# Performance work log

Hardware: AMD Instinct MI355X
Metric: run time of the kernel (lower is better)

The kernel has to match this reference:

```python
import jax, jax.numpy as jnp
import numpy as np

NUM_CLASSES = 80
PRE_NMS_K = 400    # pre_nms_points / max_output_size_per_class
MAX_BOXES = 200    # max_total_size
NMS_THRESH = 0.6
SCORE_THRESH = 0.0  # iou_thresh in YoloLayer, used as score threshold/mask
SCALE_XY = (1.2, 1.1, 1.05)  # levels 3,4,5
STRIDES = (8.0, 16.0, 32.0)  # 2**level


def setup_inputs() -> dict:
    key = jax.random.key(0)
    k3, k4, k5 = jax.random.split(key, 3)
    B, C5 = 8, 3 * (NUM_CLASSES + 5)
    p3 = jax.random.normal(k3, (B, 64, 64, C5), dtype=jnp.float32)
    p4 = jax.random.normal(k4, (B, 32, 32, C5), dtype=jnp.float32)
    p5 = jax.random.normal(k5, (B, 16, 16, C5), dtype=jnp.float32)
    a3 = jnp.array([[12., 16.], [19., 36.], [40., 28.]], jnp.float32)
    a4 = jnp.array([[36., 75.], [76., 55.], [72., 146.]], jnp.float32)
    a5 = jnp.array([[142., 110.], [192., 243.], [459., 401.]], jnp.float32)
    return {"p3": p3, "p4": p4, "p5": p5, "a3": a3, "a4": a4, "a5": a5}


def _decode_level(p, anchors, stride, scale_xy):
    # p: [B,H,W,A*(C+5)] raw head output; 'original' box decode (sigmoid xy, exp wh)
    B, H, W, _ = p.shape
    A = anchors.shape[0]
    d = p.reshape(B, H, W, A, NUM_CLASSES + 5)
    txy, twh, tobj, tcls = d[..., :2], d[..., 2:4], d[..., 4:5], d[..., 5:]
    gx, gy = jnp.meshgrid(jnp.arange(W, dtype=p.dtype), jnp.arange(H, dtype=p.dtype))
    grid = jnp.stack([gx, gy], -1)[None, :, :, None, :]          # [1,H,W,1,2] (x,y)
    sxy = jnp.asarray(scale_xy, p.dtype)
    xy = (jax.nn.sigmoid(txy) * sxy - 0.5 * (sxy - 1.0) + grid) / jnp.array([W, H], p.dtype)
    wh = jnp.exp(twh) * anchors[None, None, None] / jnp.array([W * stride, H * stride], p.dtype)
    x1y1 = xy - 0.5 * wh
    x2y2 = xy + 0.5 * wh
    boxes = jnp.stack([x1y1[..., 1], x1y1[..., 0], x2y2[..., 1], x2y2[..., 0]], -1)  # yxyx
    obj = jax.nn.sigmoid(tobj)
    cls = jax.nn.sigmoid(tcls) * obj
    N = H * W * A
    return boxes.reshape(B, N, 4), cls.reshape(B, N, NUM_CLASSES), obj.reshape(B, N)


def _pairwise_iou(b):
    # b: [K,4] yxyx in [0,1]
    area = (b[:, 2] - b[:, 0]) * (b[:, 3] - b[:, 1])
    tl = jnp.maximum(b[:, None, :2], b[None, :, :2])
    br = jnp.minimum(b[:, None, 2:], b[None, :, 2:])
    wh = jnp.maximum(br - tl, 0.0)
    inter = wh[..., 0] * wh[..., 1]
    union = area[:, None] + area[None, :] - inter
    return inter / jnp.maximum(union, 1e-9)


def _greedy_nms_scores(boxes, scores):
    # boxes/scores already sorted by score descending; returns scores with suppressed -> 0
    K = scores.shape[0]
    overlap = _pairwise_iou(boxes) > NMS_THRESH
    idx = jnp.arange(K)

    def body(i, keep):
        sup = overlap[i] & (idx > i) & keep[i]
        return keep & ~sup

    keep = jax.lax.fori_loop(0, K, body, jnp.ones((K,), bool))
    return jnp.where(keep & (scores > SCORE_THRESH), scores, 0.0)


def _detections_per_image(boxes, cls_scores):
    # boxes [N,4], cls_scores [N,C] -> combined per-class NMS, top MAX_BOXES overall
    boxes = jnp.clip(boxes, 0.0, 1.0)  # combined NMS clips boxes by default

    def per_class(scores_c):
        vals, idx = jax.lax.top_k(scores_c, PRE_NMS_K)
        b = boxes[idx]
        return _greedy_nms_scores(b, vals), b

    kept_scores, kept_boxes = jax.vmap(per_class)(cls_scores.T)  # [C,K], [C,K,4]
    flat_s = kept_scores.reshape(-1)
    flat_b = kept_boxes.reshape(-1, 4)
    cls_ids = jnp.repeat(jnp.arange(NUM_CLASSES), PRE_NMS_K)
    top_s, top_i = jax.lax.top_k(flat_s, MAX_BOXES)
    top_b = flat_b[top_i]
    top_c = cls_ids[top_i].astype(jnp.float32)
    valid = top_s > 0.0
    top_b = jnp.where(valid[:, None], top_b, 0.0)
    top_c = jnp.where(valid, top_c, 0.0)
    num = jnp.sum(valid.astype(jnp.int32))
    return top_b, top_s, top_c, num


def _forward(p3, p4, p5, a3, a4, a5):
    boxes, cls_scores, obj_scores = [], [], []
    for (p, a), stride, sxy in zip(((p3, a3), (p4, a4), (p5, a5)), STRIDES, SCALE_XY):
        b, c, o = _decode_level(p, a, stride, sxy)
        boxes.append(b); cls_scores.append(c); obj_scores.append(o)
    boxes = jnp.concatenate(boxes, 1)            # [B,N,4]
    cls_scores = jnp.concatenate(cls_scores, 1)  # [B,N,C]
    obj_scores = jnp.concatenate(obj_scores, 1)  # [B,N]
    obj_mask = (obj_scores > SCORE_THRESH).astype(boxes.dtype)
    cls_mask = (cls_scores > SCORE_THRESH).astype(boxes.dtype)
    cls_scores = cls_scores * obj_mask[..., None] * cls_mask
    return jax.vmap(_detections_per_image)(boxes, cls_scores)


def reference(p3, p4, p5, a3, a4, a5):
    bbox, confidence, classes, num_detections = _forward(p3, p4, p5, a3, a4, a5)
    return bbox, confidence, classes, num_detections
```

## Files before the change

### kernel.cpp

```cpp
#include <hip/hip_runtime.h>
#include <math.h>

#define NCLS 80
#define PRE_K 400
#define MAX_BOXES 200
#define KEEP_CAP 200
#define N_TOT 16128
#define M_FIN (NCLS * KEEP_CAP)
#define NMS_T 0.6f
#define NTHR 1024
#define NWAVE (NTHR / 64)
#define FTHR 512
#define CAP 512

typedef unsigned long long u64;
typedef unsigned int u32;
typedef unsigned short u16;

__device__ __forceinline__ float sigf(float x) { return 1.0f / (1.0f + expf(-x)); }

__device__ __forceinline__ float score_f32(int idx, int b, int c,
    const float* __restrict__ p3, const float* __restrict__ p4, const float* __restrict__ p5)
{
    const float* base; int W, n;
    if (idx < 12288)      { base = p3; W = 64; n = idx; }
    else if (idx < 15360) { base = p4; W = 32; n = idx - 12288; }
    else                  { base = p5; W = 16; n = idx - 15360; }
    int a = n % 3, hw = n / 3, w = hw % W, h = hw / W;
    const float* rec = base + (((b * W + h) * W + w) * 255 + a * 85);
    return sigf(rec[5 + c]) * sigf(rec[4]);
}

__device__ __forceinline__ void hist_agg(u32* hist, u32 d, bool valid, int lane)
{
    u64 act = __ballot(valid);
    while (act) {
        int ldr = __ffsll((unsigned long long)act) - 1;
        u32 dl = __shfl(d, ldr, 64);
        u64 m = __ballot(valid && d == dl);
        if (lane == ldr) atomicAdd(&hist[dl], (u32)__popcll(m));
        act &= ~m;
    }
}

__device__ __forceinline__ void digit_select(const u32* hist, int need,
                                             u32* sh_dg, u32* sh_S1, u32* sh_T, int tid)
{
    if (tid < 64) {
        const int lane = tid;
        u32 h0 = hist[4 * lane + 0], h1 = hist[4 * lane + 1];
        u32 h2 = hist[4 * lane + 2], h3 = hist[4 * lane + 3];
        u32 loc = h0 + h1 + h2 + h3;
        u32 s = loc;
#pragma unroll
        for (int off = 1; off < 64; off <<= 1) {
            u32 t = __shfl_down(s, off, 64);
            if (lane + off < 64) s += t;
        }
        u32 after = s - loc;
        u32 S3 = h3 + after, S2 = h2 + S3, S1v = h1 + S2, S0 = h0 + S1v;
        u32 Sarr[5] = { S0, S1v, S2, S3, after };
#pragma unroll
        for (int k = 0; k < 4; ++k) {
            if ((int)Sarr[k] >= need && need > (int)Sarr[k + 1]) {
                *sh_dg = (u32)(4 * lane + k);
                *sh_S1 = Sarr[k + 1];
                *sh_T  = Sarr[k] - Sarr[k + 1];
            }
        }
    }
    __syncthreads();
}

__device__ __forceinline__ void sort512(u64* cand, int tid)
{
    u64 v = cand[tid];
#pragma unroll
    for (int k2 = 2; k2 <= 64; k2 <<= 1) {
#pragma unroll
        for (int j = k2 >> 1; j > 0; j >>= 1) {
            u64 p = __shfl_xor(v, j, 64);
            bool takeMax = ((tid & k2) == 0) ^ ((tid & j) != 0);
            v = takeMax ? (v >= p ? v : p) : (v <= p ? v : p);
        }
    }
    for (int k2 = 128; k2 <= CAP; k2 <<= 1) {
        for (int j = k2 >> 1; j >= 64; j >>= 1) {
            __syncthreads();
            cand[tid] = v;
            __syncthreads();
            u64 p = cand[tid ^ j];
            bool takeMax = ((tid & k2) == 0) ^ ((tid & j) != 0);
            v = takeMax ? (v >= p ? v : p) : (v <= p ? v : p);
        }
#pragma unroll
        for (int j = 32; j > 0; j >>= 1) {
            u64 p = __shfl_xor(v, j, 64);
            bool takeMax = ((tid & k2) == 0) ^ ((tid & j) != 0);
            v = takeMax ? (v >= p ? v : p) : (v <= p ? v : p);
        }
    }
    __syncthreads();
    cand[tid] = v;
    __syncthreads();
}

__device__ __forceinline__ void sort512_wide(u64* cand, int tid)
{
    u64 v = 0ull;
    if (tid < 512) {
        v = cand[tid];
#pragma unroll
        for (int k2 = 2; k2 <= 64; k2 <<= 1) {
#pragma unroll
            for (int j = k2 >> 1; j > 0; j >>= 1) {
                u64 p = __shfl_xor(v, j, 64);
                bool takeMax = ((tid & k2) == 0) ^ ((tid & j) != 0);
                v = takeMax ? (v >= p ? v : p) : (v <= p ? v : p);
            }
        }
    }
    for (int k2 = 128; k2 <= CAP; k2 <<= 1) {
        for (int j = k2 >> 1; j >= 64; j >>= 1) {
            __syncthreads();
            if (tid < 512) cand[tid] = v;
            __syncthreads();
            if (tid < 512) {
                u64 p = cand[tid ^ j];
                bool takeMax = ((tid & k2) == 0) ^ ((tid & j) != 0);
                v = takeMax ? (v >= p ? v : p) : (v <= p ? v : p);
            }
        }
        if (tid < 512) {
#pragma unroll
            for (int j = 32; j > 0; j >>= 1) {
                u64 p = __shfl_xor(v, j, 64);
                bool takeMax = ((tid & k2) == 0) ^ ((tid & j) != 0);
                v = takeMax ? (v >= p ? v : p) : (v <= p ? v : p);
            }
        }
    }
    __syncthreads();
    if (tid < 512) cand[tid] = v;
    __syncthreads();
}

__global__ __launch_bounds__(256) void decode_kernel(
    const float* __restrict__ p3, const float* __restrict__ p4, const float* __restrict__ p5,
    const float* __restrict__ a3, const float* __restrict__ a4, const float* __restrict__ a5,
    u16* __restrict__ scores16, float* __restrict__ boxes)
{
    const int blk = blockIdx.x;
    const int b = blk & 7;
    const int n = ((blk >> 3) << 8) + threadIdx.x;

    const float* base; const float* anc; int logw, nn; float sx;
    if (n < 12288)      { base = p3; anc = a3; logw = 6; nn = n;         sx = 1.2f;  }
    else if (n < 15360) { base = p4; anc = a4; logw = 5; nn = n - 12288; sx = 1.1f;  }
    else                { base = p5; anc = a5; logw = 4; nn = n - 15360; sx = 1.05f; }
    const int W = 1 << logw;
    const int a = nn % 3; const int hw = nn / 3;
    const int w = hw & (W - 1); const int h = hw >> logw;
    const float winv = 1.0f / (float)W;
    const float* rec = base + ((size_t)((b * W + h) * W + w) * 255 + a * 85);

    float tx = rec[0], ty = rec[1], tw = rec[2], th = rec[3], to = rec[4];
    float sobj = sigf(to);
    float cx = (sigf(tx) * sx - 0.5f * (sx - 1.0f) + (float)w) * winv;
    float cy = (sigf(ty) * sx - 0.5f * (sx - 1.0f) + (float)h) * winv;
    float bw = expf(tw) * anc[a * 2 + 0] * (1.0f / 512.0f);
    float bh = expf(th) * anc[a * 2 + 1] * (1.0f / 512.0f);
    float x1 = cx - 0.5f * bw, x2 = cx + 0.5f * bw;
    float y1 = cy - 0.5f * bh, y2 = cy + 0.5f * bh;
    y1 = fminf(fmaxf(y1, 0.f), 1.f); x1 = fminf(fmaxf(x1, 0.f), 1.f);
    y2 = fminf(fmaxf(y2, 0.f), 1.f); x2 = fminf(fmaxf(x2, 0.f), 1.f);
    float4 bb; bb.x = y1; bb.y = x1; bb.z = y2; bb.w = x2;
    ((float4*)boxes)[b * N_TOT + n] = bb;

    u16* sb = scores16 + (long)b * NCLS * N_TOT + n;
#pragma unroll 8
    for (int cc = 0; cc < NCLS; ++cc)
        sb[(long)cc * N_TOT] = (u16)(__float_as_uint(sigf(rec[5 + cc]) * sobj) >> 16);
}

__global__ __launch_bounds__(NTHR, 2) void topk_nms_fused(
    const u16* __restrict__ scores16, const float* __restrict__ boxes,
    const float* __restrict__ p3, const float* __restrict__ p4, const float* __restrict__ p5,
    float* __restrict__ ksc, float* __restrict__ kbox)
{
    __shared__ alignas(16) u64 cand[CAP];
    __shared__ u32 hist[260];
    __shared__ u32 sh_dg, sh_S1, sh_T;
    __shared__ int sh_gcnt;
    __shared__ alignas(16) float boxbuf[5 * 448];
    __shared__ alignas(16) u64 diagbuf[64];
    __shared__ u32 keepb[16];
    __shared__ u64 sh_keptM;
    __shared__ int wpre14[14];
    __shared__ int sh_ncnt;

    float* by1 = boxbuf;
    float* bx1 = boxbuf + 448;
    float* by2 = boxbuf + 896;
    float* bx2 = boxbuf + 1344;
    float* bar = boxbuf + 1792;

    const int tid = threadIdx.x;
    const int wv = tid >> 6;
    const int lane = tid & 63;
    const int b = blockIdx.x & 7;
    const int c = blockIdx.x >> 3;

    const u16* keys16g = scores16 + (long)(b * NCLS + c) * N_TOT;
    const uint4* k4g = (const uint4*)keys16g;
    const int N8 = N_TOT >> 3;

    if (tid < 260) hist[tid] = 0u;
    if (tid == 0) sh_gcnt = 0;
    const uint4 kA = k4g[tid];
    const bool vB = (tid + NTHR) < N8;
    uint4 kB; kB.x = 0u; kB.y = 0u; kB.z = 0u; kB.w = 0u;
    if (vB) kB = k4g[tid + NTHR];
    u32 eA[8] = { kA.x & 0xffffu, kA.x >> 16, kA.y & 0xffffu, kA.y >> 16,
                  kA.z & 0xffffu, kA.z >> 16, kA.w & 0xffffu, kA.w >> 16 };
    u32 eB[8] = { kB.x & 0xffffu, kB.x >> 16, kB.y & 0xffffu, kB.y >> 16,
                  kB.z & 0xffffu, kB.z >> 16, kB.w & 0xffffu, kB.w >> 16 };
    __syncthreads();

#pragma unroll
    for (int q = 0; q < 8; ++q) hist_agg(hist, eA[q] >> 8, true, lane);
#pragma unroll
    for (int q = 0; q < 8; ++q) hist_agg(hist, eB[q] >> 8, vB, lane);
    __syncthreads();

    int need = PRE_K;
    digit_select(hist, need, &sh_dg, &sh_S1, &sh_T, tid);
    u32 thr = sh_dg; need -= (int)sh_S1;
    int C = (PRE_K - need) + (int)sh_T;
    int lvl = 1;

    if (C > CAP) {
        if (tid < 256) hist[tid] = 0u;
        __syncthreads();
#pragma unroll
        for (int q = 0; q < 8; ++q)
            if ((eA[q] >> 8) == thr) atomicAdd(&hist[eA[q] & 255u], 1u);
        if (vB) {
#pragma unroll
            for (int q = 0; q < 8; ++q)
                if ((eB[q] >> 8) == thr) atomicAdd(&hist[eB[q] & 255u], 1u);
        }
        __syncthreads();
        digit_select(hist, need, &sh_dg, &sh_S1, &sh_T, tid);
        thr = (thr << 8) | sh_dg; need -= (int)sh_S1;
        C = (PRE_K - need) + (int)sh_T;
        lvl = 2;
    }

    if (C > CAP) {
        u32 t16 = thr;
        if (tid < 256) hist[tid] = 0u;
        __syncthreads();
        for (int i = tid; i < N_TOT; i += NTHR) {
            if (keys16g[i] == (u16)t16) {
                u32 kb = __float_as_uint(score_f32(i, b, c, p3, p4, p5));
                atomicAdd(&hist[(kb >> 8) & 255u], 1u);
            }
        }
        __syncthreads();
        digit_select(hist, need, &sh_dg, &sh_S1, &sh_T, tid);
        thr = (thr << 8) | sh_dg; need -= (int)sh_S1;
        C = (PRE_K - need) + (int)sh_T;
        lvl = 3;
    }

    if (C > CAP) {
        u32 t16 = thr >> 8;
        if (tid < 256) hist[tid] = 0u;
        __syncthreads();
        for (int i = tid; i < N_TOT; i += NTHR) {
            if (keys16g[i] == (u16)t16) {
                u32 kb = __float_as_uint(score_f32(i, b, c, p3, p4, p5));
                if ((kb >> 8) == thr) atomicAdd(&hist[kb & 255u], 1u);
            }
        }
        __syncthreads();
        digit_select(hist, need, &sh_dg, &sh_S1, &sh_T, tid);
        thr = (thr << 8) | sh_dg; need -= (int)sh_S1;
        C = (PRE_K - need) + (int)sh_T;
        lvl = 4;
    }

    if (lvl <= 2) {
#pragma unroll
        for (int q = 0; q < 8; ++q) {
            bool take = (lvl == 1) ? ((eA[q] >> 8) >= thr) : (eA[q] >= thr);
            if (take) {
                int p = atomicAdd(&sh_gcnt, 1);
                int i = (tid << 3) + q;
                u32 kb = __float_as_uint(score_f32(i, b, c, p3, p4, p5));
                cand[p] = ((u64)kb << 32) | (u32)(0xFFFFFFFFu - (u32)i);
            }
        }
        if (vB) {
#pragma unroll
            for (int q = 0; q < 8; ++q) {
                bool take = (lvl == 1) ? ((eB[q] >> 8) >= thr) : (eB[q] >= thr);
                if (take) {
                    int p = atomicAdd(&sh_gcnt, 1);
                    int i = ((tid + NTHR) << 3) + q;
                    u32 kb = __float_as_uint(score_f32(i, b, c, p3, p4, p5));
                    cand[p] = ((u64)kb << 32) | (u32)(0xFFFFFFFFu - (u32)i);
                }
            }
        }
        __syncthreads();
        for (int t = C + tid; t < CAP; t += NTHR) cand[t] = 0ull;
    } else if (C <= CAP) {
        u32 t16 = (lvl == 3) ? (thr >> 8) : (thr >> 16);
        for (int i = tid; i < N_TOT; i += NTHR) {
            u32 k = keys16g[i];
            bool take = false;
            u32 kb = 0;
            if (k > t16) { take = true; kb = __float_as_uint(score_f32(i, b, c, p3, p4, p5)); }
            else if (k == t16) {
                kb = __float_as_uint(score_f32(i, b, c, p3, p4, p5));
                take = (lvl == 3) ? ((kb >> 8) >= thr) : (kb >= thr);
            }
            if (take) {
                int p = atomicAdd(&sh_gcnt, 1);
                cand[p] = ((u64)kb << 32) | (u32)(0xFFFFFFFFu - (u32)i);
            }
        }
        __syncthreads();
        for (int t = C + tid; t < CAP; t += NTHR) cand[t] = 0ull;
    } else {
        u32 t16 = thr >> 16;
        for (int i = tid; i < N_TOT; i += NTHR) {
            u32 k = keys16g[i];
            if (k < t16) continue;
            u32 kb = __float_as_uint(score_f32(i, b, c, p3, p4, p5));
            if (kb > thr) {
                int p = atomicAdd(&sh_gcnt, 1);
                cand[p] = ((u64)kb << 32) | (u32)(0xFFFFFFFFu - (u32)i);
            }
        }
        __syncthreads();
        const int G = sh_gcnt;
        u32* scr = (u32*)boxbuf;
        int lo = tid * 16; if (lo > N_TOT) lo = N_TOT;
        int hi = lo + 16;  if (hi > N_TOT) hi = N_TOT;
        int lc = 0;
        for (int i = lo; i < hi; ++i)
            if (keys16g[i] == (u16)t16 &&
                __float_as_uint(score_f32(i, b, c, p3, p4, p5)) == thr) ++lc;
        u32* sc_cur = scr; u32* sc_oth = scr + NTHR;
        sc_cur[tid] = (u32)lc;
        __syncthreads();
        for (int off = 1; off < NTHR; off <<= 1) {
            sc_oth[tid] = sc_cur[tid] + ((tid >= off) ? sc_cur[tid - off] : 0u);
            __syncthreads();
            u32* tmp = sc_cur; sc_cur = sc_oth; sc_oth = tmp;
        }
        int r = (int)sc_cur[tid] - lc;
        for (int i = lo; i < hi; ++i) {
            if (keys16g[i] == (u16)t16 &&
                __float_as_uint(score_f32(i, b, c, p3, p4, p5)) == thr) {
                if (r < need) cand[G + r] = ((u64)thr << 32) | (u32)(0xFFFFFFFFu - (u32)i);
                ++r;
            }
        }
        __syncthreads();
        for (int t = PRE_K + tid; t < CAP; t += NTHR) cand[t] = 0ull;
    }
    __syncthreads();

    sort512_wide(cand, tid);

    const float4* btab = (const float4*)boxes;
    for (int t = tid; t < 448; t += NTHR) {
        float y1 = 0.f, x1 = 0.f, y2 = 0.f, x2 = 0.f;
        if (t < PRE_K) {
            u64 key = cand[t];
            if ((key >> 32) != 0ull) {
                int idx = (int)(0xFFFFFFFFu - (u32)(key & 0xFFFFFFFFull));
                float4 bb = btab[b * N_TOT + idx];
                y1 = bb.x; x1 = bb.y; y2 = bb.z; x2 = bb.w;
            }
        }
        by1[t] = y1; bx1[t] = x1; by2[t] = y2; bx2[t] = x2;
        bar[t] = (y2 - y1) * (x2 - x1);
    }
    if (tid < 16) keepb[tid] = (tid < 12) ? 0xFFFFFFFFu : ((tid == 12) ? 0xFFFFu : 0u);
    __syncthreads();

    for (int ch = 0; ch < 7; ++ch) {
        const int rbase = ch << 6;
        const float ry1 = by1[rbase + lane], rx1v = bx1[rbase + lane];
        const float ry2 = by2[rbase + lane], rx2v = bx2[rbase + lane];
        const float ra  = bar[rbase + lane];

#pragma unroll
        for (int q = 0; q < 4; ++q) {
            const int jl = wv * 4 + q;
            const int jj = rbase + jl;
            u64 m = 0ull;
            if (jj < PRE_K && ((keepb[jj >> 5] >> (jj & 31)) & 1u)) {
                float cy1 = by1[jj], cx1 = bx1[jj], cy2 = by2[jj], cx2 = bx2[jj], ca = bar[jj];
                float ty = fmaxf(ry1, cy1), tx = fmaxf(rx1v, cx1);
                float byv = fminf(ry2, cy2), rxv = fminf(rx2v, cx2);
                float inter = fmaxf(byv - ty, 0.f) * fmaxf(rxv - tx, 0.f);
                float uni = ra + ca - inter;
                bool o = (lane < jl) && ((inter / fmaxf(uni, 1e-9f)) > NMS_T);
                m = __ballot(o);
            }
            if (lane == 0) diagbuf[jl] = m;
        }
        __syncthreads();

        if (tid < 64) {
            u64 dg = diagbuf[lane];
            int ri = rbase + lane;
            int alive = (ri < PRE_K) ? (int)((keepb[ri >> 5] >> (ri & 31)) & 1u) : 0;
            u64 M = __ballot(alive != 0);
            for (int i = 0; i < 64; ++i) {
                if ((M >> i) & 1ull) {
                    int kill = (int)((dg >> i) & 1ull);
                    alive &= ~kill;
                    M = __ballot(alive != 0);
                }
            }
            if (lane == 0) {
                sh_keptM = M;
                keepb[2 * ch]     = (u32)(M & 0xFFFFFFFFull);
                keepb[2 * ch + 1] = (u32)(M >> 32);
            }
        }
        __syncthreads();

        {
            const u64 keptM = sh_keptM;
            if (keptM != 0ull) {
                for (int jj = rbase + 64 + wv; jj < PRE_K; jj += NWAVE) {
                    if ((keepb[jj >> 5] >> (jj & 31)) & 1u) {
                        float cy1 = by1[jj], cx1 = bx1[jj], cy2 = by2[jj], cx2 = bx2[jj], ca = bar[jj];
                        float ty = fmaxf(ry1, cy1), tx = fmaxf(rx1v, cx1);
                        float byv = fminf(ry2, cy2), rxv = fminf(rx2v, cx2);
                        float inter = fmaxf(byv - ty, 0.f) * fmaxf(rxv - tx, 0.f);
                        float uni = ra + ca - inter;
                        bool o = (inter / fmaxf(uni, 1e-9f)) > NMS_T;
                        u64 m = __ballot(o);
                        if ((m & keptM) != 0ull && lane == 0)
                            atomicAnd(&keepb[jj >> 5], ~(1u << (jj & 31)));
                    }
                }
            }
        }
        __syncthreads();
    }

    if (tid == 0) {
        int acc = 0;
        for (int w = 0; w < 14; ++w) { wpre14[w] = acc; acc += __popc(keepb[w]); }
        sh_ncnt = acc < KEEP_CAP ? acc : KEEP_CAP;
    }
    __syncthreads();

    const int blk_out = b * NCLS + c;
    float* osc = ksc + (long)blk_out * KEEP_CAP;
    float* obx = kbox + (long)blk_out * KEEP_CAP * 4;
    for (int t = tid; t < PRE_K; t += NTHR) {
        u32 kw = keepb[t >> 5];
        if ((kw >> (t & 31)) & 1u) {
            int pos = wpre14[t >> 5] + __popc(kw & ((1u << (t & 31)) - 1u));
            if (pos < KEEP_CAP) {
                osc[pos] = __uint_as_float((u32)(cand[t] >> 32));
                obx[pos * 4 + 0] = by1[t]; obx[pos * 4 + 1] = bx1[t];
                obx[pos * 4 + 2] = by2[t]; obx[pos * 4 + 3] = bx2[t];
            }
        }
    }
    for (int t = sh_ncnt + tid; t < KEEP_CAP; t += NTHR) {
        osc[t] = 0.0f;
        obx[t * 4 + 0] = 0.f; obx[t * 4 + 1] = 0.f;
        obx[t * 4 + 2] = 0.f; obx[t * 4 + 3] = 0.f;
    }
}

__device__ __forceinline__ void radix_topk_sort_f32(
    const u32* __restrict__ keys, int n, int K,
    u64* cand, u32* hist, u32* scr,
    u32* sh_dg, u32* sh_S1, u32* sh_T, int* sh_gcnt, int tid)
{
    int need = K;
    digit_select(hist, need, sh_dg, sh_S1, sh_T, tid);
    u32 thr = *sh_dg; need -= (int)*sh_S1;
    int C = (K - need) + (int)*sh_T;
    int eshift = 24;

    const uint4* k4 = (const uint4*)keys;
    const int n4 = n >> 2;
    const int nIter = (n4 + FTHR - 1) / FTHR;

    for (int shift = 16; shift >= 0 && C > CAP; shift -= 8) {
        if (tid < 256) hist[tid] = 0u;
        __syncthreads();
        for (int it = 0; it < nIter; ++it) {
            int i4 = tid + it * FTHR;
            if (i4 < n4) {
                uint4 kk = k4[i4];
                if ((kk.x >> (shift + 8)) == thr) atomicAdd(&hist[(kk.x >> shift) & 255u], 1u);
                if ((kk.y >> (shift + 8)) == thr) atomicAdd(&hist[(kk.y >> shift) & 255u], 1u);
                if ((kk.z >> (shift + 8)) == thr) atomicAdd(&hist[(kk.z >> shift) & 255u], 1u);
                if ((kk.w >> (shift + 8)) == thr) atomicAdd(&hist[(kk.w >> shift) & 255u], 1u);
            }
        }
        __syncthreads();
        digit_select(hist, need, sh_dg, sh_S1, sh_T, tid);
        thr = (thr << 8) | *sh_dg; need -= (int)*sh_S1;
        C = (K - need) + (int)*sh_T;
        eshift = shift;
    }

    if (C <= CAP) {
        for (int it = 0; it < nIter; ++it) {
            int i4 = tid + it * FTHR;
            if (i4 < n4) {
                uint4 kk = k4[i4];
                int i0 = i4 << 2;
                if ((kk.x >> eshift) >= thr) { int p = atomicAdd(sh_gcnt, 1); cand[p] = ((u64)kk.x << 32) | (u32)(0xFFFFFFFFu - (u32)(i0 + 0)); }
                if ((kk.y >> eshift) >= thr) { int p = atomicAdd(sh_gcnt, 1); cand[p] = ((u64)kk.y << 32) | (u32)(0xFFFFFFFFu - (u32)(i0 + 1)); }
                if ((kk.z >> eshift) >= thr) { int p = atomicAdd(sh_gcnt, 1); cand[p] = ((u64)kk.z << 32) | (u32)(0xFFFFFFFFu - (u32)(i0 + 2)); }
                if ((kk.w >> eshift) >= thr) { int p = atomicAdd(sh_gcnt, 1); cand[p] = ((u64)kk.w << 32) | (u32)(0xFFFFFFFFu - (u32)(i0 + 3)); }
            }
        }
        __syncthreads();
        for (int t = C + tid; t < CAP; t += FTHR) cand[t] = 0ull;
    } else {
        for (int i = tid; i < n; i += FTHR) {
            u32 k = keys[i];
            if (k > thr) {
                int p = atomicAdd(sh_gcnt, 1);
                cand[p] = ((u64)k << 32) | (u32)(0xFFFFFFFFu - (u32)i);
            }
        }
        __syncthreads();
        const int G = *sh_gcnt;
        int lo = tid * 32; if (lo > n) lo = n;
        int hi = lo + 32;  if (hi > n) hi = n;
        int lc = 0;
        for (int i = lo; i < hi; ++i) if (keys[i] == thr) ++lc;
        u32* sc_cur = scr; u32* sc_oth = scr + 512;
        sc_cur[tid] = (u32)lc;
        __syncthreads();
        for (int off = 1; off < FTHR; off <<= 1) {
            sc_oth[tid] = sc_cur[tid] + ((tid >= off) ? sc_cur[tid - off] : 0u);
            __syncthreads();
            u32* tmp = sc_cur; sc_cur = sc_oth; sc_oth = tmp;
        }
        int r = (int)sc_cur[tid] - lc;
        for (int i = lo; i < hi; ++i) {
            if (keys[i] == thr) {
                if (r < need) cand[G + r] = ((u64)thr << 32) | (u32)(0xFFFFFFFFu - (u32)i);
                ++r;
            }
        }
        __syncthreads();
        for (int t = K + tid; t < CAP; t += FTHR) cand[t] = 0ull;
    }
    __syncthreads();
    sort512(cand, tid);
}

__global__ __launch_bounds__(FTHR) void final_topk_kernel(
    const float* __restrict__ ksc, const float* __restrict__ kbox,
    float* __restrict__ out)
{
    __shared__ alignas(16) u64 cand[CAP];
    __shared__ u32 hist[260];
    __shared__ u32 scr[1024];
    __shared__ u32 sh_dg, sh_S1, sh_T;
    __shared__ int sh_gcnt;

    const int tid = threadIdx.x;
    const int lane = tid & 63;
    const int b = blockIdx.x;
    const u32* keys = (const u32*)(ksc + (long)b * M_FIN);

    if (tid < 260) hist[tid] = 0u;
    if (tid == 0) sh_gcnt = 0;
    __syncthreads();
    const uint4* k4 = (const uint4*)keys;
#pragma unroll
    for (int it = 0; it < 8; ++it) {
        int i4 = tid + it * FTHR;
        bool v = i4 < (M_FIN >> 2);
        u32 d0 = 0, d1 = 0, d2 = 0, d3 = 0;
        if (v) {
            uint4 kk = k4[i4];
            d0 = kk.x >> 24; d1 = kk.y >> 24; d2 = kk.z >> 24; d3 = kk.w >> 24;
        }
        hist_agg(hist, d0, v, lane);
        hist_agg(hist, d1, v, lane);
        hist_agg(hist, d2, v, lane);
        hist_agg(hist, d3, v, lane);
    }
    __syncthreads();

    radix_topk_sort_f32(keys, M_FIN, MAX_BOXES, cand, hist, scr,
                        &sh_dg, &sh_S1, &sh_T, &sh_gcnt, tid);

    float* obb = out;
    float* ocf = out + 8 * MAX_BOXES * 4;
    float* ocl = ocf + 8 * MAX_BOXES;
    float* onm = ocl + 8 * MAX_BOXES;

    float s = 0.f;
    if (tid < MAX_BOXES) {
        u64 key = cand[tid];
        s = __uint_as_float((u32)(key >> 32));
        float y1 = 0.f, x1 = 0.f, y2 = 0.f, x2 = 0.f, cid = 0.f;
        if (s > 0.0f) {
            int i = (int)(0xFFFFFFFFu - (u32)(key & 0xFFFFFFFFull));
            int cc = i / KEEP_CAP, j = i % KEEP_CAP;
            const float* bb = kbox + (((long)b * NCLS + cc) * KEEP_CAP + j) * 4;
            y1 = bb[0]; x1 = bb[1]; y2 = bb[2]; x2 = bb[3];
            cid = (float)cc;
        }
        long o = (long)b * MAX_BOXES + tid;
        obb[o * 4 + 0] = y1; obb[o * 4 + 1] = x1; obb[o * 4 + 2] = y2; obb[o * 4 + 3] = x2;
        ocf[o] = s; ocl[o] = cid;
    }
    int cnt = __syncthreads_count(tid < MAX_BOXES && s > 0.0f);
    if (tid == 0) onm[b] = (float)cnt;
}

extern "C" void kernel_launch(void* const* d_in, const int* in_sizes, int n_in,
                              void* d_out, int out_size, void* d_ws, size_t ws_size,
                              hipStream_t stream) {
    const float* p3 = (const float*)d_in[0];
    const float* p4 = (const float*)d_in[1];
    const float* p5 = (const float*)d_in[2];
    const float* a3 = (const float*)d_in[3];
    const float* a4 = (const float*)d_in[4];
    const float* a5 = (const float*)d_in[5];
    float* out = (float*)d_out;

    const size_t s16_bytes  = (size_t)8 * NCLS * N_TOT * 2;
    const size_t box_bytes  = (size_t)8 * N_TOT * 16;
    const size_t ksc_bytes  = (size_t)8 * NCLS * KEEP_CAP * 4;

    u16*   scores16 = (u16*)d_ws;
    float* boxes    = (float*)((char*)d_ws + s16_bytes);
    float* ksc      = (float*)((char*)d_ws + s16_bytes + box_bytes);
    float* kbox     = (float*)((char*)d_ws + s16_bytes + box_bytes + ksc_bytes);

    decode_kernel<<<504, 256, 0, stream>>>(p3, p4, p5, a3, a4, a5, scores16, boxes);
    topk_nms_fused<<<8 * NCLS, NTHR, 0, stream>>>(scores16, boxes, p3, p4, p5, ksc, kbox);
    final_topk_kernel<<<8, FTHR, 0, stream>>>(ksc, kbox, out);
}
```

Baseline: 179.4 us.

## Replace atomic histogram with ballot bit-matching and branchless NMS chunk scan

The first-level radix histogram in both the per-class top-k kernel and the final top-k kernel is now built with six ballots per element. Each lane counts the elements matching its own 6-bit digit, and per-wave counts are summed in a new 64-bin digit select. This replaces the leader-loop shared-memory atomics. It relies on scores being non-negative and below 1, so the top byte fits in 6 bits. The NMS suppression matrix is also transposed so each row holds the boxes it suppresses, and the serial 64-step keep resolution becomes a branchless shuffle-and-mask loop instead of repeated ballots.

```diff
diff --git a/kernel.cpp b/kernel.cpp
--- a/kernel.cpp
+++ b/kernel.cpp
@@ -31,18 +31,6 @@
     return sigf(rec[5 + c]) * sigf(rec[4]);
 }
 
-__device__ __forceinline__ void hist_agg(u32* hist, u32 d, bool valid, int lane)
-{
-    u64 act = __ballot(valid);
-    while (act) {
-        int ldr = __ffsll((unsigned long long)act) - 1;
-        u32 dl = __shfl(d, ldr, 64);
-        u64 m = __ballot(valid && d == dl);
-        if (lane == ldr) atomicAdd(&hist[dl], (u32)__popcll(m));
-        act &= ~m;
-    }
-}
-
 __device__ __forceinline__ void digit_select(const u32* hist, int need,
                                              u32* sh_dg, u32* sh_S1, u32* sh_T, int tid)
 {
@@ -67,6 +55,28 @@
                 *sh_S1 = Sarr[k + 1];
                 *sh_T  = Sarr[k] - Sarr[k + 1];
             }
+        }
+    }
+    __syncthreads();
+}
+
+__device__ __forceinline__ void digit_select64(const u32* histw, int nwaves, int need,
+                                               u32* sh_dg, u32* sh_S1, u32* sh_T, int tid)
+{
+    if (tid < 64) {
+        const int lane = tid;
+        u32 tot = 0;
+        for (int w = 0; w < nwaves; ++w) tot += histw[w * 64 + lane];
+        u32 s = tot;
+#pragma unroll
+        for (int off = 1; off < 64; off <<= 1) {
+            u32 t = __shfl_down(s, off, 64);
+            if (lane + off < 64) s += t;
+        }
+        u32 Sd1 = __shfl_down(s, 1, 64);
+        if (lane == 63) Sd1 = 0;
+        if ((int)s >= need && need > (int)Sd1) {
+            *sh_dg = (u32)lane; *sh_S1 = Sd1; *sh_T = tot;
         }
     }
     __syncthreads();
@@ -190,6 +200,7 @@
 {
     __shared__ alignas(16) u64 cand[CAP];
     __shared__ u32 hist[260];
+    __shared__ u32 histw[NWAVE * 64];
     __shared__ u32 sh_dg, sh_S1, sh_T;
     __shared__ int sh_gcnt;
     __shared__ alignas(16) float boxbuf[5 * 448];
@@ -215,7 +226,6 @@
     const uint4* k4g = (const uint4*)keys16g;
     const int N8 = N_TOT >> 3;
 
-    if (tid < 260) hist[tid] = 0u;
     if (tid == 0) sh_gcnt = 0;
     const uint4 kA = k4g[tid];
     const bool vB = (tid + NTHR) < N8;
@@ -225,16 +235,41 @@
                   kA.z & 0xffffu, kA.z >> 16, kA.w & 0xffffu, kA.w >> 16 };
     u32 eB[8] = { kB.x & 0xffffu, kB.x >> 16, kB.y & 0xffffu, kB.y >> 16,
                   kB.z & 0xffffu, kB.z >> 16, kB.w & 0xffffu, kB.w >> 16 };
-    __syncthreads();
-
-#pragma unroll
-    for (int q = 0; q < 8; ++q) hist_agg(hist, eA[q] >> 8, true, lane);
-#pragma unroll
-    for (int q = 0; q < 8; ++q) hist_agg(hist, eB[q] >> 8, vB, lane);
+
+    {
+        u64 inv[6];
+#pragma unroll
+        for (int k = 0; k < 6; ++k) inv[k] = ((lane >> k) & 1) ? 0ull : ~0ull;
+        u32 cnt = 0;
+#pragma unroll
+        for (int r = 0; r < 8; ++r) {
+            u32 d = eA[r] >> 8;
+            u64 macc = ~0ull;
+#pragma unroll
+            for (int k = 0; k < 6; ++k) {
+                u64 bk = __ballot(((d >> k) & 1) != 0);
+                macc &= (bk ^ inv[k]);
+            }
+            cnt += (u32)__popcll(macc);
+        }
+        const u64 mv = __ballot(vB);
+#pragma unroll
+        for (int r = 0; r < 8; ++r) {
+            u32 d = eB[r] >> 8;
+            u64 macc = mv;
+#pragma unroll
+            for (int k = 0; k < 6; ++k) {
+                u64 bk = __ballot(((d >> k) & 1) != 0);
+                macc &= (bk ^ inv[k]);
+            }
+            cnt += (u32)__popcll(macc);
+        }
+        histw[wv * 64 + lane] = cnt;
+    }
     __syncthreads();
 
     int need = PRE_K;
-    digit_select(hist, need, &sh_dg, &sh_S1, &sh_T, tid);
+    digit_select64(histw, NWAVE, need, &sh_dg, &sh_S1, &sh_T, tid);
     u32 thr = sh_dg; need -= (int)sh_S1;
     int C = (PRE_K - need) + (int)sh_T;
     int lvl = 1;
@@ -402,38 +437,36 @@
 
 #pragma unroll
         for (int q = 0; q < 4; ++q) {
-            const int jl = wv * 4 + q;
-            const int jj = rbase + jl;
+            const int rl = wv * 4 + q;
+            const int rr = rbase + rl;
             u64 m = 0ull;
-            if (jj < PRE_K && ((keepb[jj >> 5] >> (jj & 31)) & 1u)) {
-                float cy1 = by1[jj], cx1 = bx1[jj], cy2 = by2[jj], cx2 = bx2[jj], ca = bar[jj];
-                float ty = fmaxf(ry1, cy1), tx = fmaxf(rx1v, cx1);
-                float byv = fminf(ry2, cy2), rxv = fminf(rx2v, cx2);
+            bool rowAlive = (rr < PRE_K) && ((keepb[rr >> 5] >> (rr & 31)) & 1u);
+            if (rowAlive) {
+                float qy1 = by1[rr], qx1 = bx1[rr], qy2 = by2[rr], qx2 = bx2[rr], qa = bar[rr];
+                float ty = fmaxf(qy1, ry1), tx = fmaxf(qx1, rx1v);
+                float byv = fminf(qy2, ry2), rxv = fminf(qx2, rx2v);
                 float inter = fmaxf(byv - ty, 0.f) * fmaxf(rxv - tx, 0.f);
-                float uni = ra + ca - inter;
-                bool o = (lane < jl) && ((inter / fmaxf(uni, 1e-9f)) > NMS_T);
+                float uni = qa + ra - inter;
+                bool o = (lane > rl) && ((inter / fmaxf(uni, 1e-9f)) > NMS_T);
                 m = __ballot(o);
             }
-            if (lane == 0) diagbuf[jl] = m;
+            if (lane == 0) diagbuf[rl] = m;
         }
         __syncthreads();
 
         if (tid < 64) {
-            u64 dg = diagbuf[lane];
-            int ri = rbase + lane;
-            int alive = (ri < PRE_K) ? (int)((keepb[ri >> 5] >> (ri & 31)) & 1u) : 0;
-            u64 M = __ballot(alive != 0);
+            u64 dgrow = diagbuf[lane];
+            u64 kept = ((u64)keepb[2 * ch + 1] << 32) | (u64)keepb[2 * ch];
+#pragma unroll 16
             for (int i = 0; i < 64; ++i) {
-                if ((M >> i) & 1ull) {
-                    int kill = (int)((dg >> i) & 1ull);
-                    alive &= ~kill;
-                    M = __ballot(alive != 0);
-                }
+                u64 dgi = __shfl(dgrow, i);
+                u64 msk = 0ull - ((kept >> i) & 1ull);
+                kept &= ~(dgi & msk);
             }
             if (lane == 0) {
-                sh_keptM = M;
-                keepb[2 * ch]     = (u32)(M & 0xFFFFFFFFull);
-                keepb[2 * ch + 1] = (u32)(M >> 32);
+                sh_keptM = kept;
+                keepb[2 * ch]     = (u32)(kept & 0xFFFFFFFFull);
+                keepb[2 * ch + 1] = (u32)(kept >> 32);
             }
         }
         __syncthreads();
@@ -489,13 +522,10 @@
 
 __device__ __forceinline__ void radix_topk_sort_f32(
     const u32* __restrict__ keys, int n, int K,
+    u32 thr, int need, int C,
     u64* cand, u32* hist, u32* scr,
     u32* sh_dg, u32* sh_S1, u32* sh_T, int* sh_gcnt, int tid)
 {
-    int need = K;
-    digit_select(hist, need, sh_dg, sh_S1, sh_T, tid);
-    u32 thr = *sh_dg; need -= (int)*sh_S1;
-    int C = (K - need) + (int)*sh_T;
     int eshift = 24;
 
     const uint4* k4 = (const uint4*)keys;
@@ -583,31 +613,48 @@
     __shared__ int sh_gcnt;
 
     const int tid = threadIdx.x;
+    const int wv = tid >> 6;
     const int lane = tid & 63;
     const int b = blockIdx.x;
     const u32* keys = (const u32*)(ksc + (long)b * M_FIN);
 
-    if (tid < 260) hist[tid] = 0u;
     if (tid == 0) sh_gcnt = 0;
-    __syncthreads();
     const uint4* k4 = (const uint4*)keys;
-#pragma unroll
-    for (int it = 0; it < 8; ++it) {
-        int i4 = tid + it * FTHR;
-        bool v = i4 < (M_FIN >> 2);
-        u32 d0 = 0, d1 = 0, d2 = 0, d3 = 0;
-        if (v) {
-            uint4 kk = k4[i4];
-            d0 = kk.x >> 24; d1 = kk.y >> 24; d2 = kk.z >> 24; d3 = kk.w >> 24;
-        }
-        hist_agg(hist, d0, v, lane);
-        hist_agg(hist, d1, v, lane);
-        hist_agg(hist, d2, v, lane);
-        hist_agg(hist, d3, v, lane);
-    }
-    __syncthreads();
-
-    radix_topk_sort_f32(keys, M_FIN, MAX_BOXES, cand, hist, scr,
+
+    {
+        u64 inv[6];
+#pragma unroll
+        for (int k = 0; k < 6; ++k) inv[k] = ((lane >> k) & 1) ? 0ull : ~0ull;
+        u32 cnt = 0;
+#pragma unroll
+        for (int it = 0; it < 8; ++it) {
+            int i4 = tid + it * FTHR;
+            bool v = i4 < (M_FIN >> 2);
+            uint4 kk; kk.x = 0u; kk.y = 0u; kk.z = 0u; kk.w = 0u;
+            if (v) kk = k4[i4];
+            u64 mv = __ballot(v);
+            u32 ds[4] = { kk.x >> 24, kk.y >> 24, kk.z >> 24, kk.w >> 24 };
+#pragma unroll
+            for (int q = 0; q < 4; ++q) {
+                u64 macc = mv;
+#pragma unroll
+                for (int k = 0; k < 6; ++k) {
+                    u64 bk = __ballot(((ds[q] >> k) & 1) != 0);
+                    macc &= (bk ^ inv[k]);
+                }
+                cnt += (u32)__popcll(macc);
+            }
+        }
+        scr[wv * 64 + lane] = cnt;
+    }
+    __syncthreads();
+
+    int need = MAX_BOXES;
+    digit_select64(scr, FTHR / 64, need, &sh_dg, &sh_S1, &sh_T, tid);
+    u32 thr = sh_dg; need -= (int)sh_S1;
+    int C = (MAX_BOXES - need) + (int)sh_T;
+
+    radix_topk_sort_f32(keys, M_FIN, MAX_BOXES, thr, need, C, cand, hist, scr,
                         &sh_dg, &sh_S1, &sh_T, &sh_gcnt, tid);
 
     float* obb = out;
```

Measured after the change: 184.7 us. +3.0%, slower.
